# Optimization experiments

Measured on AMD Instinct MI355X. Metric: run time of the kernel, lower is better.

Reference implementation:

```python
import jax, jax.numpy as jnp
import numpy as np

VAR_SCALE = 0.1


def setup_inputs() -> dict:
    key = jax.random.key(0)
    k_x, k_tc, k_task, k_in, k_out = jax.random.split(key, 5)
    B, T, IN, OUT, R = 1024, 8, 4096, 4096, 64
    x = jax.random.normal(k_x, (B, T, IN), dtype=jnp.float32)
    tensor_core = jax.random.normal(k_tc, (R, R, R), dtype=jnp.float32) * VAR_SCALE
    task_core = jax.random.normal(k_task, (T, R), dtype=jnp.float32) * VAR_SCALE
    in_core = jax.random.normal(k_in, (IN, R), dtype=jnp.float32) * VAR_SCALE
    out_core = jax.random.normal(k_out, (OUT, R), dtype=jnp.float32) * VAR_SCALE
    return {"x": x, "tensor_core": tensor_core, "task_core": task_core,
            "in_core": in_core, "out_core": out_core}


def reference(x, tensor_core, task_core, in_core, out_core):
    # Tucker weight reconstruction, faithful to the torch einsum chain.
    # W1: [T, R, R] = task_core @ tensor_core (contract first core mode)
    W = jnp.einsum('tj,jkl->tkl', task_core, tensor_core)
    # W2: [T, IN, R] = contract in_core with middle mode
    W = jnp.einsum('ij,tjk->tik', in_core, W)
    # W3: [T, IN, OUT] = contract out_core with last mode
    W = jnp.einsum('oj,tij->tio', out_core, W)
    # Batched per-task matmul: x [B, T, IN] -> y [B, T, OUT]
    y = jnp.einsum('bti,tio->bto', x, W)
    return y
```

## Files before the change

kernel.cpp:

```cpp
#include <hip/hip_runtime.h>
#include <hip/hip_bf16.h>


typedef __bf16 bf16;
typedef __bf16 bf16x8 __attribute__((ext_vector_type(8)));
typedef __bf16 bf16x4 __attribute__((ext_vector_type(4)));
typedef float  f32x4  __attribute__((ext_vector_type(4)));

__device__ __forceinline__ bf16x8 load_frag_bf16(const bf16* p) {
    return *reinterpret_cast<const bf16x8*>(p);
}

__device__ __forceinline__ bf16x8 load_frag_f32(const float* p) {
    f32x4 a = *reinterpret_cast<const f32x4*>(p);
    f32x4 b = *reinterpret_cast<const f32x4*>(p + 4);
    bf16x8 r;
    r[0] = (bf16)a[0]; r[1] = (bf16)a[1]; r[2] = (bf16)a[2]; r[3] = (bf16)a[3];
    r[4] = (bf16)b[0]; r[5] = (bf16)b[1]; r[6] = (bf16)b[2]; r[7] = (bf16)b[3];
    return r;
}

__device__ __forceinline__ f32x4 mfma16(bf16x8 a, bf16x8 b, f32x4 c) {
    return __builtin_amdgcn_mfma_f32_16x16x32_bf16(a, b, c, 0, 0, 0);
}

__global__ __launch_bounds__(256) void k1_w1(
    const float* __restrict__ task,
    const float* __restrict__ tensor,
    bf16* __restrict__ w1)
{
    int t    = blockIdx.x >> 4;
    int part = blockIdx.x & 15;
    int idx  = part * 256 + threadIdx.x;
    int j    = idx >> 6;
    int k    = idx & 63;
    float acc = 0.f;
    #pragma unroll 8
    for (int m = 0; m < 64; ++m)
        acc += task[t * 64 + m] * tensor[(m * 64 + j) * 64 + k];
    w1[(t * 64 + j) * 64 + k] = (bf16)acc;
}

__global__ __launch_bounds__(256) void kt_ict(
    const float* __restrict__ in_core,
    bf16* __restrict__ icT)
{
    int idx = blockIdx.x * 256 + threadIdx.x;
    int i0  = (idx & 511) * 8;
    int j   = idx >> 9;
    bf16x8 v;
    #pragma unroll
    for (int s = 0; s < 8; ++s)
        v[s] = (bf16)in_core[(size_t)(i0 + s) * 64 + j];
    *reinterpret_cast<bf16x8*>(icT + (size_t)j * 4096 + i0) = v;
}

__global__ __launch_bounds__(256) void k2_mt(
    const float* __restrict__ out_core,
    const bf16* __restrict__ w1,
    bf16* __restrict__ mt)
{
    int t    = blockIdx.x >> 6;
    int ot   = blockIdx.x & 63;
    int wave = threadIdx.x >> 6;
    int lane = threadIdx.x & 63;
    int m    = lane & 15;
    int q    = lane >> 4;
    int o0   = ot * 64 + wave * 16;

    f32x4 acc[4] = {};
    #pragma unroll
    for (int kc = 0; kc < 64; kc += 32) {
        bf16x8 a = load_frag_f32(out_core + (size_t)(o0 + m) * 64 + kc + q * 8);
        #pragma unroll
        for (int nt = 0; nt < 4; ++nt) {
            bf16x8 b = load_frag_bf16(w1 + (size_t)(t * 64 + nt * 16 + m) * 64 + kc + q * 8);
            acc[nt] = mfma16(a, b, acc[nt]);
        }
    }
    #pragma unroll
    for (int nt = 0; nt < 4; ++nt) {
        #pragma unroll
        for (int r = 0; r < 4; ++r) {
            int o = o0 + q * 4 + r;
            mt[(size_t)(t * 4096 + o) * 64 + nt * 16 + m] = (bf16)acc[nt][r];
        }
    }
}

__global__ __launch_bounds__(256) void k0_z(
    const float* __restrict__ x,
    const bf16* __restrict__ icT,
    float* __restrict__ pp,
    int kchunk)
{
    __shared__ bf16 xs[16 * 256];
    int ks       = blockIdx.x >> 9;
    int mt       = blockIdx.x & 511;
    int row_base = mt * 16;
    int kbeg     = ks * kchunk;
    int tid  = threadIdx.x;
    int r    = tid >> 4;
    int c16  = tid & 15;
    int wave = tid >> 6;
    int lane = tid & 63;
    int m    = lane & 15;
    int q    = lane >> 4;
    int n0   = wave * 16;

    const float* gsrc = x   + (size_t)(row_base + r) * 4096 + kbeg;
    const bf16*  bbas = icT + (size_t)(n0 + m) * 4096 + kbeg;

    f32x4 v[4];
    #pragma unroll
    for (int i = 0; i < 4; ++i)
        v[i] = *reinterpret_cast<const f32x4*>(gsrc + c16 * 4 + i * 64);

    f32x4 acc = {};
    for (int kc = 0; kc < kchunk; kc += 256) {
        __syncthreads();
        #pragma unroll
        for (int i = 0; i < 4; ++i) {
            bf16x4 w;
            w[0] = (bf16)v[i][0]; w[1] = (bf16)v[i][1];
            w[2] = (bf16)v[i][2]; w[3] = (bf16)v[i][3];
            int col = c16 * 4 + i * 64;
            int u   = (col >> 3) ^ (r & 7);
            *reinterpret_cast<bf16x4*>(&xs[r * 256 + u * 8 + (col & 7)]) = w;
        }
        __syncthreads();
        if (kc + 256 < kchunk) {
            #pragma unroll
            for (int i = 0; i < 4; ++i)
                v[i] = *reinterpret_cast<const f32x4*>(gsrc + kc + 256 + c16 * 4 + i * 64);
        }
        #pragma unroll
        for (int c = 0; c < 8; ++c) {
            int u = (c * 4 + q) ^ (m & 7);
            bf16x8 a = *reinterpret_cast<const bf16x8*>(&xs[m * 256 + u * 8]);
            bf16x8 b = load_frag_bf16(bbas + kc + c * 32 + q * 8);
            acc = mfma16(a, b, acc);
        }
    }
    float* dst = pp + (size_t)ks * 524288 + (size_t)row_base * 64;
    #pragma unroll
    for (int rr = 0; rr < 4; ++rr)
        dst[(q * 4 + rr) * 64 + n0 + m] = acc[rr];
}

__global__ __launch_bounds__(256) void k_reduce(
    const float* __restrict__ pp,
    bf16* __restrict__ z,
    int nsplit)
{
    int idx = (blockIdx.x * 256 + threadIdx.x) * 4;
    f32x4 s = *reinterpret_cast<const f32x4*>(pp + idx);
    for (int sp = 1; sp < nsplit; ++sp)
        s += *reinterpret_cast<const f32x4*>(pp + (size_t)sp * 524288 + idx);
    bf16x4 o;
    o[0] = (bf16)s[0]; o[1] = (bf16)s[1]; o[2] = (bf16)s[2]; o[3] = (bf16)s[3];
    *reinterpret_cast<bf16x4*>(z + idx) = o;
}

__global__ __launch_bounds__(256) void k3_y(
    const bf16* __restrict__ z,
    const bf16* __restrict__ mt,
    float* __restrict__ y)
{
    __shared__ float slab[4 * 2112];
    int bx    = blockIdx.x;
    int t     = bx >> 8;
    int rest  = bx & 255;
    int mtile = rest >> 5;
    int ntile = rest & 31;
    int wave  = threadIdx.x >> 6;
    int lane  = threadIdx.x & 63;
    int m     = lane & 15;
    int q     = lane >> 4;

    int b_base = mtile * 128 + wave * 32;
    int n_base = ntile * 128;

    f32x4 acc[2][8] = {};
    #pragma unroll
    for (int kc = 0; kc < 64; kc += 32) {
        bf16x8 a0 = load_frag_bf16(z + (size_t)((b_base + m) * 8 + t) * 64 + kc + q * 8);
        bf16x8 a1 = load_frag_bf16(z + (size_t)((b_base + 16 + m) * 8 + t) * 64 + kc + q * 8);
        #pragma unroll
        for (int nt = 0; nt < 8; ++nt) {
            bf16x8 b = load_frag_bf16(mt + (size_t)(t * 4096 + n_base + nt * 16 + m) * 64 + kc + q * 8);
            acc[0][nt] = mfma16(a0, b, acc[0][nt]);
            acc[1][nt] = mfma16(a1, b, acc[1][nt]);
        }
    }

    float* sw = slab + wave * 2112;
    #pragma unroll
    for (int sub = 0; sub < 2; ++sub) {
        #pragma unroll
        for (int nt = 0; nt < 8; ++nt) {
            #pragma unroll
            for (int r = 0; r < 4; ++r)
                sw[(q * 4 + r) * 132 + nt * 16 + m] = acc[sub][nt][r];
        }
        __syncthreads();
        #pragma unroll
        for (int p = 0; p < 8; ++p) {
            int row = 2 * p + (lane >> 5);
            int cu  = lane & 31;
            f32x4 d = *reinterpret_cast<const f32x4*>(sw + row * 132 + cu * 4);
            int b   = b_base + sub * 16 + row;
            *reinterpret_cast<f32x4*>(y + (size_t)(b * 8 + t) * 4096 + n_base + cu * 4) = d;
        }
        __syncthreads();
    }
}

extern "C" void kernel_launch(void* const* d_in, const int* in_sizes, int n_in,
                              void* d_out, int out_size, void* d_ws, size_t ws_size,
                              hipStream_t stream) {
    const float* x        = (const float*)d_in[0];
    const float* tensor_c = (const float*)d_in[1];
    const float* task_c   = (const float*)d_in[2];
    const float* in_c     = (const float*)d_in[3];
    const float* out_c    = (const float*)d_in[4];
    float* y = (float*)d_out;

    char* ws = (char*)d_ws;
    bf16*  w1  = (bf16*)ws;
    bf16*  icT = (bf16*)(ws + (64 << 10));
    bf16*  mtc = (bf16*)(ws + (64 << 10) + (512 << 10));
    bf16*  zb  = (bf16*)(ws + (64 << 10) + (512 << 10) + (4 << 20));
    float* pp  = (float*)(ws + (64 << 10) + (512 << 10) + (4 << 20) + (1 << 20));

    size_t fixed = (size_t)(64 << 10) + (512 << 10) + (4 << 20) + (1 << 20);
    int KS = 4;
    while (KS > 1 && fixed + (size_t)KS * 2097152 > ws_size) KS >>= 1;
    int kchunk = 4096 / KS;

    k1_w1   <<<128,      256, 0, stream>>>(task_c, tensor_c, w1);
    kt_ict  <<<128,      256, 0, stream>>>(in_c, icT);
    k2_mt   <<<512,      256, 0, stream>>>(out_c, w1, mtc);
    k0_z    <<<512 * KS, 256, 0, stream>>>(x, icT, pp, kchunk);
    k_reduce<<<512,      256, 0, stream>>>(pp, zb, KS);
    k3_y    <<<2048,     256, 0, stream>>>(zb, mtc, y);
}
```

Baseline: 285.4 us.

## Drop split-K for the x projection and merge the setup kernels

```diff
diff --git a/kernel.cpp b/kernel.cpp
--- a/kernel.cpp
+++ b/kernel.cpp
@@ -24,35 +24,34 @@
     return __builtin_amdgcn_mfma_f32_16x16x32_bf16(a, b, c, 0, 0, 0);
 }
 
-__global__ __launch_bounds__(256) void k1_w1(
+__global__ __launch_bounds__(256) void k_setup(
     const float* __restrict__ task,
     const float* __restrict__ tensor,
-    bf16* __restrict__ w1)
-{
-    int t    = blockIdx.x >> 4;
-    int part = blockIdx.x & 15;
-    int idx  = part * 256 + threadIdx.x;
-    int j    = idx >> 6;
-    int k    = idx & 63;
-    float acc = 0.f;
-    #pragma unroll 8
-    for (int m = 0; m < 64; ++m)
-        acc += task[t * 64 + m] * tensor[(m * 64 + j) * 64 + k];
-    w1[(t * 64 + j) * 64 + k] = (bf16)acc;
-}
-
-__global__ __launch_bounds__(256) void kt_ict(
     const float* __restrict__ in_core,
+    bf16* __restrict__ w1,
     bf16* __restrict__ icT)
 {
-    int idx = blockIdx.x * 256 + threadIdx.x;
-    int i0  = (idx & 511) * 8;
-    int j   = idx >> 9;
-    bf16x8 v;
-    #pragma unroll
-    for (int s = 0; s < 8; ++s)
-        v[s] = (bf16)in_core[(size_t)(i0 + s) * 64 + j];
-    *reinterpret_cast<bf16x8*>(icT + (size_t)j * 4096 + i0) = v;
+    int bid = blockIdx.x;
+    if (bid < 128) {
+        int t    = bid >> 4;
+        int idx  = (bid & 15) * 256 + threadIdx.x;
+        int j    = idx >> 6;
+        int k    = idx & 63;
+        float acc = 0.f;
+        #pragma unroll 8
+        for (int m = 0; m < 64; ++m)
+            acc += task[t * 64 + m] * tensor[(m * 64 + j) * 64 + k];
+        w1[(t * 64 + j) * 64 + k] = (bf16)acc;
+    } else {
+        int idx = (bid - 128) * 256 + threadIdx.x;
+        int i0  = (idx & 511) * 8;
+        int j   = idx >> 9;
+        bf16x8 v;
+        #pragma unroll
+        for (int s = 0; s < 8; ++s)
+            v[s] = (bf16)in_core[(size_t)(i0 + s) * 64 + j];
+        *reinterpret_cast<bf16x8*>(icT + (size_t)j * 4096 + i0) = v;
+    }
 }
 
 __global__ __launch_bounds__(256) void k2_mt(
@@ -91,14 +90,10 @@
 __global__ __launch_bounds__(256) void k0_z(
     const float* __restrict__ x,
     const bf16* __restrict__ icT,
-    float* __restrict__ pp,
-    int kchunk)
+    bf16* __restrict__ z)
 {
     __shared__ bf16 xs[16 * 256];
-    int ks       = blockIdx.x >> 9;
-    int mt       = blockIdx.x & 511;
-    int row_base = mt * 16;
-    int kbeg     = ks * kchunk;
+    int row_base = blockIdx.x * 16;
     int tid  = threadIdx.x;
     int r    = tid >> 4;
     int c16  = tid & 15;
@@ -108,31 +103,35 @@
     int q    = lane >> 4;
     int n0   = wave * 16;
 
-    const float* gsrc = x   + (size_t)(row_base + r) * 4096 + kbeg;
-    const bf16*  bbas = icT + (size_t)(n0 + m) * 4096 + kbeg;
-
-    f32x4 v[4];
+    const float* gsrc = x   + (size_t)(row_base + r) * 4096;
+    const bf16*  bbas = icT + (size_t)(n0 + m) * 4096;
+
+    f32x4 vA[4], vB[4];
     #pragma unroll
     for (int i = 0; i < 4; ++i)
-        v[i] = *reinterpret_cast<const f32x4*>(gsrc + c16 * 4 + i * 64);
+        vA[i] = *reinterpret_cast<const f32x4*>(gsrc + c16 * 4 + i * 64);
+    #pragma unroll
+    for (int i = 0; i < 4; ++i)
+        vB[i] = *reinterpret_cast<const f32x4*>(gsrc + 256 + c16 * 4 + i * 64);
 
     f32x4 acc = {};
-    for (int kc = 0; kc < kchunk; kc += 256) {
+    #pragma unroll 1
+    for (int kc = 0; kc < 4096; kc += 512) {
         __syncthreads();
         #pragma unroll
         for (int i = 0; i < 4; ++i) {
             bf16x4 w;
-            w[0] = (bf16)v[i][0]; w[1] = (bf16)v[i][1];
-            w[2] = (bf16)v[i][2]; w[3] = (bf16)v[i][3];
+            w[0] = (bf16)vA[i][0]; w[1] = (bf16)vA[i][1];
+            w[2] = (bf16)vA[i][2]; w[3] = (bf16)vA[i][3];
             int col = c16 * 4 + i * 64;
             int u   = (col >> 3) ^ (r & 7);
             *reinterpret_cast<bf16x4*>(&xs[r * 256 + u * 8 + (col & 7)]) = w;
         }
         __syncthreads();
-        if (kc + 256 < kchunk) {
+        if (kc + 512 < 4096) {
             #pragma unroll
             for (int i = 0; i < 4; ++i)
-                v[i] = *reinterpret_cast<const f32x4*>(gsrc + kc + 256 + c16 * 4 + i * 64);
+                vA[i] = *reinterpret_cast<const f32x4*>(gsrc + kc + 512 + c16 * 4 + i * 64);
         }
         #pragma unroll
         for (int c = 0; c < 8; ++c) {
@@ -141,25 +140,34 @@
             bf16x8 b = load_frag_bf16(bbas + kc + c * 32 + q * 8);
             acc = mfma16(a, b, acc);
         }
-    }
-    float* dst = pp + (size_t)ks * 524288 + (size_t)row_base * 64;
+        __syncthreads();
+        #pragma unroll
+        for (int i = 0; i < 4; ++i) {
+            bf16x4 w;
+            w[0] = (bf16)vB[i][0]; w[1] = (bf16)vB[i][1];
+            w[2] = (bf16)vB[i][2]; w[3] = (bf16)vB[i][3];
+            int col = c16 * 4 + i * 64;
+            int u   = (col >> 3) ^ (r & 7);
+            *reinterpret_cast<bf16x4*>(&xs[r * 256 + u * 8 + (col & 7)]) = w;
+        }
+        __syncthreads();
+        if (kc + 768 < 4096) {
+            #pragma unroll
+            for (int i = 0; i < 4; ++i)
+                vB[i] = *reinterpret_cast<const f32x4*>(gsrc + kc + 768 + c16 * 4 + i * 64);
+        }
+        #pragma unroll
+        for (int c = 0; c < 8; ++c) {
+            int u = (c * 4 + q) ^ (m & 7);
+            bf16x8 a = *reinterpret_cast<const bf16x8*>(&xs[m * 256 + u * 8]);
+            bf16x8 b = load_frag_bf16(bbas + kc + 256 + c * 32 + q * 8);
+            acc = mfma16(a, b, acc);
+        }
+    }
+    bf16* dst = z + (size_t)row_base * 64;
     #pragma unroll
     for (int rr = 0; rr < 4; ++rr)
-        dst[(q * 4 + rr) * 64 + n0 + m] = acc[rr];
-}
-
-__global__ __launch_bounds__(256) void k_reduce(
-    const float* __restrict__ pp,
-    bf16* __restrict__ z,
-    int nsplit)
-{
-    int idx = (blockIdx.x * 256 + threadIdx.x) * 4;
-    f32x4 s = *reinterpret_cast<const f32x4*>(pp + idx);
-    for (int sp = 1; sp < nsplit; ++sp)
-        s += *reinterpret_cast<const f32x4*>(pp + (size_t)sp * 524288 + idx);
-    bf16x4 o;
-    o[0] = (bf16)s[0]; o[1] = (bf16)s[1]; o[2] = (bf16)s[2]; o[3] = (bf16)s[3];
-    *reinterpret_cast<bf16x4*>(z + idx) = o;
+        dst[(q * 4 + rr) * 64 + n0 + m] = (bf16)acc[rr];
 }
 
 __global__ __launch_bounds__(256) void k3_y(
@@ -203,7 +211,6 @@
             for (int r = 0; r < 4; ++r)
                 sw[(q * 4 + r) * 132 + nt * 16 + m] = acc[sub][nt][r];
         }
-        __syncthreads();
         #pragma unroll
         for (int p = 0; p < 8; ++p) {
             int row = 2 * p + (lane >> 5);
@@ -212,7 +219,6 @@
             int b   = b_base + sub * 16 + row;
             *reinterpret_cast<f32x4*>(y + (size_t)(b * 8 + t) * 4096 + n_base + cu * 4) = d;
         }
-        __syncthreads();
     }
 }
 
@@ -227,21 +233,13 @@
     float* y = (float*)d_out;
 
     char* ws = (char*)d_ws;
-    bf16*  w1  = (bf16*)ws;
-    bf16*  icT = (bf16*)(ws + (64 << 10));
-    bf16*  mtc = (bf16*)(ws + (64 << 10) + (512 << 10));
-    bf16*  zb  = (bf16*)(ws + (64 << 10) + (512 << 10) + (4 << 20));
-    float* pp  = (float*)(ws + (64 << 10) + (512 << 10) + (4 << 20) + (1 << 20));
-
-    size_t fixed = (size_t)(64 << 10) + (512 << 10) + (4 << 20) + (1 << 20);
-    int KS = 4;
-    while (KS > 1 && fixed + (size_t)KS * 2097152 > ws_size) KS >>= 1;
-    int kchunk = 4096 / KS;
-
-    k1_w1   <<<128,      256, 0, stream>>>(task_c, tensor_c, w1);
-    kt_ict  <<<128,      256, 0, stream>>>(in_c, icT);
-    k2_mt   <<<512,      256, 0, stream>>>(out_c, w1, mtc);
-    k0_z    <<<512 * KS, 256, 0, stream>>>(x, icT, pp, kchunk);
-    k_reduce<<<512,      256, 0, stream>>>(pp, zb, KS);
-    k3_y    <<<2048,     256, 0, stream>>>(zb, mtc, y);
-}
+    bf16* w1  = (bf16*)ws;
+    bf16* icT = (bf16*)(ws + (64 << 10));
+    bf16* mtc = (bf16*)(ws + (64 << 10) + (512 << 10));
+    bf16* zb  = (bf16*)(ws + (64 << 10) + (512 << 10) + (4 << 20));
+
+    k_setup<<<256,  256, 0, stream>>>(task_c, tensor_c, in_c, w1, icT);
+    k2_mt  <<<512,  256, 0, stream>>>(out_c, w1, mtc);
+    k0_z   <<<512,  256, 0, stream>>>(x, icT, zb);
+    k3_y   <<<2048, 256, 0, stream>>>(zb, mtc, y);
+}
```

New measurement: 281.2 us. No clear change (-1.5%).
